# Performance work log

Hardware: AMD Instinct MI355X
Metric: run time of the kernel (lower is better)

Reference implementation:

```python
import jax, jax.numpy as jnp
import numpy as np

EPS = 1e-4

def safe_clamp(x, max_val):
    # nan -> 0, +inf -> max_val, -inf -> -max_val, then clamp to [-max_val, max_val]
    x = jnp.where(jnp.isnan(x), 0.0, x)
    x = jnp.where(jnp.isinf(x) & (x > 0), max_val, x)
    x = jnp.where(jnp.isinf(x) & (x < 0), -max_val, x)
    return jnp.clip(x, -max_val, max_val)

def setup_inputs() -> dict:
    key = jax.random.key(0)
    k1, k2 = jax.random.split(key)
    hidden_states = jax.random.normal(k1, (4, 4096, 2048), dtype=jnp.float32)
    ln_weight = jnp.ones((2048,), dtype=jnp.float32)
    ln_bias = jnp.zeros((2048,), dtype=jnp.float32)
    gate_weight = jax.random.normal(k2, (64, 2048), dtype=jnp.float32) * 0.01
    return {"hidden_states": hidden_states, "ln_weight": ln_weight,
            "ln_bias": ln_bias, "gate_weight": gate_weight}

def reference(hidden_states, ln_weight, ln_bias, gate_weight):
    B, S, H = hidden_states.shape
    top_k = 2
    x = hidden_states.reshape(-1, H)  # (N, H)
    # LayerNorm(eps=1e-5)
    mu = jnp.mean(x, axis=-1, keepdims=True)
    var = jnp.mean((x - mu) ** 2, axis=-1, keepdims=True)
    x = (x - mu) * jax.lax.rsqrt(var + 1e-5) * ln_weight + ln_bias
    x = safe_clamp(x, 50.0)
    # gate: (N, H) @ (H, E)
    router_logits = jnp.clip(x @ gate_weight.T, -10.0, 10.0)
    # eval mode: no noise
    router_probs = jnp.clip(jax.nn.softmax(router_logits, axis=-1), EPS, 1.0)
    top_k_probs, top_k_indices = jax.lax.top_k(router_probs, top_k)
    prob_sum = jnp.maximum(jnp.sum(top_k_probs, axis=-1, keepdims=True), EPS)
    top_k_probs = top_k_probs / prob_sum
    return top_k_probs, top_k_indices, router_logits
```

## Files before the change

### kernel.cpp

```cpp
#include <hip/hip_runtime.h>
#include <math.h>

#define H 2048
#define E 64
#define MR 16
#define NCH 16
#define LR 136

typedef _Float16 half8  __attribute__((ext_vector_type(8)));
typedef _Float16 half4h __attribute__((ext_vector_type(4)));
typedef float    f32x4  __attribute__((ext_vector_type(4)));

#define MFMA16(A,B,C) __builtin_amdgcn_mfma_f32_16x16x32_f16(A,B,C,0,0,0)


__global__ __launch_bounds__(256) void prep_fused(const float* __restrict__ W,
        const float* __restrict__ lnw, const float* __restrict__ lnb,
        _Float16* __restrict__ Bh, _Float16* __restrict__ Bl,
        float* __restrict__ csum, float* __restrict__ bsum) {
    {
        int idx  = blockIdx.x * 256 + threadIdx.x;
        int lane = idx & 63;
        int e  = ((idx >> 6) & 3) * 16 + (lane & 15);
        int k0 = (idx >> 8) * 32 + ((lane >> 4) << 3);
        half8 hh, ll;
        #pragma unroll
        for (int j = 0; j < 8; ++j) {
            float wf = lnw[k0 + j] * W[e * H + k0 + j];
            _Float16 h = (_Float16)wf;
            _Float16 l = (_Float16)((wf - (float)h) * 2048.0f);
            hh[j] = h; ll[j] = l;
        }
        *(half8*)&Bh[(long)idx * 8] = hh;
        *(half8*)&Bl[(long)idx * 8] = ll;
    }
    {
        __shared__ float rc[256], rb[256];
        int e = blockIdx.x, t = threadIdx.x;
        float cs = 0.f, bs = 0.f;
        #pragma unroll
        for (int j = 0; j < 8; ++j) {
            int k = t + j * 256;
            float w = W[e * H + k];
            cs += lnw[k] * w;
            bs += lnb[k] * w;
        }
        rc[t] = cs; rb[t] = bs;
        __syncthreads();
        for (int s = 128; s > 0; s >>= 1) {
            if (t < s) { rc[t] += rc[t + s]; rb[t] += rb[t + s]; }
            __syncthreads();
        }
        if (t == 0) { csum[e] = rc[0]; bsum[e] = rb[0]; }
    }
}

__global__ __launch_bounds__(256, 4) void router_kernel(
    const float* __restrict__ X, const _Float16* __restrict__ Bh,
    const _Float16* __restrict__ Bl, const float* __restrict__ csum,
    const float* __restrict__ bsum, float* __restrict__ out, int nRows)
{
    __shared__ __align__(16) _Float16 Xh[2][MR][LR];
    __shared__ __align__(16) _Float16 Xl[2][MR][LR];
    __shared__ float C2[MR][E + 4];
    __shared__ float mu_s[MR], rs_s[MR];

    const int t    = threadIdx.x;
    const int lane = t & 63;
    const int et   = t >> 6;
    const int q    = lane >> 4;
    const int ln16 = lane & 15;
    const int rowR = t >> 4;
    const int cS   = t & 15;
    const long rowBase = (long)blockIdx.x * MR;
    const long iOff = (long)nRows * 2;
    const long lOff = (long)nRows * 4;

    const float4* Xrow = (const float4*)X + (rowBase + rowR) * 512;

    float sacc = 0.f, qacc = 0.f;
    f32x4 acc0 = (f32x4)0.f;
    f32x4 acc1 = (f32x4)0.f;

    half8 WAh0, WAh1, WAh2, WAh3, WAl0, WAl1, WAl2, WAl3;
    half8 WBh0, WBh1, WBh2, WBh3, WBl0, WBl1, WBl2, WBl3;
    float4 vA0, vA1, vB0, vB1;

#define LOADW(S, c) { \
    int b0_ = ((((c) * 4 + 0) * 4 + et) * 64 + lane) * 8; \
    S##h0 = *(const half8*)&Bh[b0_];  S##l0 = *(const half8*)&Bl[b0_]; \
    int b1_ = ((((c) * 4 + 1) * 4 + et) * 64 + lane) * 8; \
    S##h1 = *(const half8*)&Bh[b1_];  S##l1 = *(const half8*)&Bl[b1_]; \
    int b2_ = ((((c) * 4 + 2) * 4 + et) * 64 + lane) * 8; \
    S##h2 = *(const half8*)&Bh[b2_];  S##l2 = *(const half8*)&Bl[b2_]; \
    int b3_ = ((((c) * 4 + 3) * 4 + et) * 64 + lane) * 8; \
    S##h3 = *(const half8*)&Bh[b3_];  S##l3 = *(const half8*)&Bl[b3_]; }

#define LOADX(S, c) { \
    S##0 = Xrow[(c) * 32 + cS]; \
    S##1 = Xrow[(c) * 32 + cS + 16]; }

#define CVT1(V, JCOL, buf) { \
    float4 v_ = (V); \
    sacc += v_.x + v_.y + v_.z + v_.w; \
    qacc += v_.x * v_.x + v_.y * v_.y + v_.z * v_.z + v_.w * v_.w; \
    _Float16 h0_ = (_Float16)v_.x, h1_ = (_Float16)v_.y, \
             h2_ = (_Float16)v_.z, h3_ = (_Float16)v_.w; \
    _Float16 l0_ = (_Float16)((v_.x - (float)h0_) * 2048.f); \
    _Float16 l1_ = (_Float16)((v_.y - (float)h1_) * 2048.f); \
    _Float16 l2_ = (_Float16)((v_.z - (float)h2_) * 2048.f); \
    _Float16 l3_ = (_Float16)((v_.w - (float)h3_) * 2048.f); \
    half4h hh_ = {h0_, h1_, h2_, h3_}; \
    half4h ll_ = {l0_, l1_, l2_, l3_}; \
    *(half4h*)&Xh[buf][rowR][(JCOL) * 4] = hh_; \
    *(half4h*)&Xl[buf][rowR][(JCOL) * 4] = ll_; }

#define CONVERT(S, buf) { CVT1(S##0, cS, buf) CVT1(S##1, cS + 16, buf) }

#define MFMAKS(Wh_, Wl_, buf, ks) { \
    half8 Ah_ = *(const half8*)&Xh[buf][ln16][(ks) * 32 + q * 8]; \
    half8 Al_ = *(const half8*)&Xl[buf][ln16][(ks) * 32 + q * 8]; \
    acc0 = MFMA16(Ah_, Wh_, acc0); \
    acc1 = MFMA16(Ah_, Wl_, acc1); \
    acc1 = MFMA16(Al_, Wh_, acc1); }

#define MFMAC(S, buf) { \
    MFMAKS(S##h0, S##l0, buf, 0) MFMAKS(S##h1, S##l1, buf, 1) \
    MFMAKS(S##h2, S##l2, buf, 2) MFMAKS(S##h3, S##l3, buf, 3) }

    {
        float4 v00 = Xrow[cS];
        float4 v01 = Xrow[cS + 16];
        LOADW(WA, 0)
        LOADX(vA, 1)
        CVT1(v00, cS, 0)
        CVT1(v01, cS + 16, 0)
    }
    __syncthreads();

    for (int c = 0; c < NCH; c += 2) {
        LOADW(WB, c + 1)
        if (c + 2 < NCH) LOADX(vB, c + 2)
        MFMAC(WA, 0)
        CONVERT(vA, 1)
        __syncthreads();

        if (c + 2 < NCH) LOADW(WA, c + 2)
        if (c + 3 < NCH) LOADX(vA, c + 3)
        MFMAC(WB, 1)
        if (c + 2 < NCH) CONVERT(vB, 0)
        __syncthreads();
    }

    {
        float s = sacc, qq = qacc;
        #pragma unroll
        for (int d = 1; d < 16; d <<= 1) {
            s  += __shfl_xor(s, d);
            qq += __shfl_xor(qq, d);
        }
        if (cS == 0) {
            float mu  = s * (1.f / H);
            float var = qq * (1.f / H) - mu * mu;
            mu_s[rowR] = mu;
            rs_s[rowR] = rsqrtf(var + 1e-5f);
        }
    }
    __syncthreads();

    {
        int n = et * 16 + ln16;
        float cs = csum[n], bs = bsum[n];
        #pragma unroll
        for (int reg = 0; reg < 4; ++reg) {
            int r = q * 4 + reg;
            float raw = acc0[reg] + acc1[reg] * (1.f / 2048.f);
            float lg = rs_s[r] * (raw - mu_s[r] * cs) + bs;
            lg = fminf(fmaxf(lg, -10.f), 10.f);
            out[lOff + (rowBase + r) * 64 + n] = lg;
            C2[r][n] = lg;
        }
    }
    __syncthreads();

    #pragma unroll
    for (int rr = 0; rr < 4; ++rr) {
        int r = et * 4 + rr;
        float l = C2[r][lane];
        float m = l;
        #pragma unroll
        for (int d = 1; d < 64; d <<= 1) m = fmaxf(m, __shfl_xor(m, d));
        float p = __expf(l - m);
        float ssum = p;
        #pragma unroll
        for (int d = 1; d < 64; d <<= 1) ssum += __shfl_xor(ssum, d);
        float prob = fminf(fmaxf(p / ssum, 1e-4f), 1.0f);

        float v1 = prob; int i1 = lane;
        #pragma unroll
        for (int d = 1; d < 64; d <<= 1) {
            float ov = __shfl_xor(v1, d);
            int   oi = __shfl_xor(i1, d);
            if (ov > v1 || (ov == v1 && oi < i1)) { v1 = ov; i1 = oi; }
        }
        float v2 = (lane == i1) ? -1.f : prob; int i2 = lane;
        #pragma unroll
        for (int d = 1; d < 64; d <<= 1) {
            float ov = __shfl_xor(v2, d);
            int   oi = __shfl_xor(i2, d);
            if (ov > v2 || (ov == v2 && oi < i2)) { v2 = ov; i2 = oi; }
        }
        if (lane == 0) {
            float ps = fmaxf(v1 + v2, 1e-4f);
            long rg_ = rowBase + r;
            out[rg_ * 2 + 0] = v1 / ps;
            out[rg_ * 2 + 1] = v2 / ps;
            out[iOff + rg_ * 2 + 0] = (float)i1;
            out[iOff + rg_ * 2 + 1] = (float)i2;
        }
    }
}

extern "C" void kernel_launch(void* const* d_in, const int* in_sizes, int n_in,
                              void* d_out, int out_size, void* d_ws, size_t ws_size,
                              hipStream_t stream) {
    const float* X   = (const float*)d_in[0];
    const float* lnw = (const float*)d_in[1];
    const float* lnb = (const float*)d_in[2];
    const float* W   = (const float*)d_in[3];
    float* outp = (float*)d_out;

    _Float16* Bh = (_Float16*)d_ws;
    _Float16* Bl = Bh + H * E;
    float* csum  = (float*)(Bl + H * E);
    float* bsum  = csum + E;

    int N = in_sizes[0] / H;

    prep_fused<<<64, 256, 0, stream>>>(W, lnw, lnb, Bh, Bl, csum, bsum);
    router_kernel<<<N / MR, 256, 0, stream>>>(X, Bh, Bl, csum, bsum, outp, N);
}
```

Before: 244.6 us.

## Load X fragments directly into registers, drop LDS staging and barriers

Each wave now reads its MFMA A-operand rows of X directly from global memory and splits them into fp16 hi/lo parts in registers, removing the LDS double buffer and per-chunk block barriers. LayerNorm statistics are reduced with cross-lane shuffles instead of shared memory. This eliminates LDS traffic and synchronization, but all four waves now redundantly load and convert the same X rows with a less coalesced row-strided pattern, and the occupancy hint is dropped.

```diff
diff --git a/kernel.cpp b/kernel.cpp
--- a/kernel.cpp
+++ b/kernel.cpp
@@ -4,11 +4,9 @@
 #define H 2048
 #define E 64
 #define MR 16
-#define NCH 16
-#define LR 136
+#define NKS 64
 
 typedef _Float16 half8  __attribute__((ext_vector_type(8)));
-typedef _Float16 half4h __attribute__((ext_vector_type(4)));
 typedef float    f32x4  __attribute__((ext_vector_type(4)));
 
 #define MFMA16(A,B,C) __builtin_amdgcn_mfma_f32_16x16x32_f16(A,B,C,0,0,0)
@@ -55,118 +53,100 @@
     }
 }
 
-__global__ __launch_bounds__(256, 4) void router_kernel(
+__global__ __launch_bounds__(256) void router_kernel(
     const float* __restrict__ X, const _Float16* __restrict__ Bh,
     const _Float16* __restrict__ Bl, const float* __restrict__ csum,
     const float* __restrict__ bsum, float* __restrict__ out, int nRows)
 {
-    __shared__ __align__(16) _Float16 Xh[2][MR][LR];
-    __shared__ __align__(16) _Float16 Xl[2][MR][LR];
     __shared__ float C2[MR][E + 4];
-    __shared__ float mu_s[MR], rs_s[MR];
 
     const int t    = threadIdx.x;
     const int lane = t & 63;
     const int et   = t >> 6;
     const int q    = lane >> 4;
     const int ln16 = lane & 15;
-    const int rowR = t >> 4;
-    const int cS   = t & 15;
     const long rowBase = (long)blockIdx.x * MR;
     const long iOff = (long)nRows * 2;
     const long lOff = (long)nRows * 4;
 
-    const float4* Xrow = (const float4*)X + (rowBase + rowR) * 512;
-
-    float sacc = 0.f, qacc = 0.f;
+    const float4* Xp = (const float4*)X + (rowBase + ln16) * 512 + q * 2;
+    const half8* BhP = (const half8*)Bh + et * 64 + lane;
+    const half8* BlP = (const half8*)Bl + et * 64 + lane;
+
     f32x4 acc0 = (f32x4)0.f;
     f32x4 acc1 = (f32x4)0.f;
-
-    half8 WAh0, WAh1, WAh2, WAh3, WAl0, WAl1, WAl2, WAl3;
-    half8 WBh0, WBh1, WBh2, WBh3, WBl0, WBl1, WBl2, WBl3;
-    float4 vA0, vA1, vB0, vB1;
-
-#define LOADW(S, c) { \
-    int b0_ = ((((c) * 4 + 0) * 4 + et) * 64 + lane) * 8; \
-    S##h0 = *(const half8*)&Bh[b0_];  S##l0 = *(const half8*)&Bl[b0_]; \
-    int b1_ = ((((c) * 4 + 1) * 4 + et) * 64 + lane) * 8; \
-    S##h1 = *(const half8*)&Bh[b1_];  S##l1 = *(const half8*)&Bl[b1_]; \
-    int b2_ = ((((c) * 4 + 2) * 4 + et) * 64 + lane) * 8; \
-    S##h2 = *(const half8*)&Bh[b2_];  S##l2 = *(const half8*)&Bl[b2_]; \
-    int b3_ = ((((c) * 4 + 3) * 4 + et) * 64 + lane) * 8; \
-    S##h3 = *(const half8*)&Bh[b3_];  S##l3 = *(const half8*)&Bl[b3_]; }
-
-#define LOADX(S, c) { \
-    S##0 = Xrow[(c) * 32 + cS]; \
-    S##1 = Xrow[(c) * 32 + cS + 16]; }
-
-#define CVT1(V, JCOL, buf) { \
-    float4 v_ = (V); \
-    sacc += v_.x + v_.y + v_.z + v_.w; \
-    qacc += v_.x * v_.x + v_.y * v_.y + v_.z * v_.z + v_.w * v_.w; \
-    _Float16 h0_ = (_Float16)v_.x, h1_ = (_Float16)v_.y, \
-             h2_ = (_Float16)v_.z, h3_ = (_Float16)v_.w; \
-    _Float16 l0_ = (_Float16)((v_.x - (float)h0_) * 2048.f); \
-    _Float16 l1_ = (_Float16)((v_.y - (float)h1_) * 2048.f); \
-    _Float16 l2_ = (_Float16)((v_.z - (float)h2_) * 2048.f); \
-    _Float16 l3_ = (_Float16)((v_.w - (float)h3_) * 2048.f); \
-    half4h hh_ = {h0_, h1_, h2_, h3_}; \
-    half4h ll_ = {l0_, l1_, l2_, l3_}; \
-    *(half4h*)&Xh[buf][rowR][(JCOL) * 4] = hh_; \
-    *(half4h*)&Xl[buf][rowR][(JCOL) * 4] = ll_; }
-
-#define CONVERT(S, buf) { CVT1(S##0, cS, buf) CVT1(S##1, cS + 16, buf) }
-
-#define MFMAKS(Wh_, Wl_, buf, ks) { \
-    half8 Ah_ = *(const half8*)&Xh[buf][ln16][(ks) * 32 + q * 8]; \
-    half8 Al_ = *(const half8*)&Xl[buf][ln16][(ks) * 32 + q * 8]; \
-    acc0 = MFMA16(Ah_, Wh_, acc0); \
-    acc1 = MFMA16(Ah_, Wl_, acc1); \
-    acc1 = MFMA16(Al_, Wh_, acc1); }
-
-#define MFMAC(S, buf) { \
-    MFMAKS(S##h0, S##l0, buf, 0) MFMAKS(S##h1, S##l1, buf, 1) \
-    MFMAKS(S##h2, S##l2, buf, 2) MFMAKS(S##h3, S##l3, buf, 3) }
-
-    {
-        float4 v00 = Xrow[cS];
-        float4 v01 = Xrow[cS + 16];
-        LOADW(WA, 0)
-        LOADX(vA, 1)
-        CVT1(v00, cS, 0)
-        CVT1(v01, cS + 16, 0)
-    }
-    __syncthreads();
-
-    for (int c = 0; c < NCH; c += 2) {
-        LOADW(WB, c + 1)
-        if (c + 2 < NCH) LOADX(vB, c + 2)
-        MFMAC(WA, 0)
-        CONVERT(vA, 1)
-        __syncthreads();
-
-        if (c + 2 < NCH) LOADW(WA, c + 2)
-        if (c + 3 < NCH) LOADX(vA, c + 3)
-        MFMAC(WB, 1)
-        if (c + 2 < NCH) CONVERT(vB, 0)
-        __syncthreads();
-    }
-
-    {
-        float s = sacc, qq = qacc;
-        #pragma unroll
-        for (int d = 1; d < 16; d <<= 1) {
-            s  += __shfl_xor(s, d);
-            qq += __shfl_xor(qq, d);
-        }
-        if (cS == 0) {
-            float mu  = s * (1.f / H);
-            float var = qq * (1.f / H) - mu * mu;
-            mu_s[rowR] = mu;
-            rs_s[rowR] = rsqrtf(var + 1e-5f);
-        }
-    }
-    __syncthreads();
+    float sacc = 0.f, qacc = 0.f;
+
+#define CVT8(V0, V1, AH, AL) { \
+    float4 v0_ = (V0), v1_ = (V1); \
+    sacc += v0_.x + v0_.y + v0_.z + v0_.w + v1_.x + v1_.y + v1_.z + v1_.w; \
+    qacc += v0_.x*v0_.x + v0_.y*v0_.y + v0_.z*v0_.z + v0_.w*v0_.w \
+          + v1_.x*v1_.x + v1_.y*v1_.y + v1_.z*v1_.z + v1_.w*v1_.w; \
+    _Float16 h0_ = (_Float16)v0_.x, h1_ = (_Float16)v0_.y, \
+             h2_ = (_Float16)v0_.z, h3_ = (_Float16)v0_.w, \
+             h4_ = (_Float16)v1_.x, h5_ = (_Float16)v1_.y, \
+             h6_ = (_Float16)v1_.z, h7_ = (_Float16)v1_.w; \
+    AH[0] = h0_; AH[1] = h1_; AH[2] = h2_; AH[3] = h3_; \
+    AH[4] = h4_; AH[5] = h5_; AH[6] = h6_; AH[7] = h7_; \
+    AL[0] = (_Float16)((v0_.x - (float)h0_) * 2048.f); \
+    AL[1] = (_Float16)((v0_.y - (float)h1_) * 2048.f); \
+    AL[2] = (_Float16)((v0_.z - (float)h2_) * 2048.f); \
+    AL[3] = (_Float16)((v0_.w - (float)h3_) * 2048.f); \
+    AL[4] = (_Float16)((v1_.x - (float)h4_) * 2048.f); \
+    AL[5] = (_Float16)((v1_.y - (float)h5_) * 2048.f); \
+    AL[6] = (_Float16)((v1_.z - (float)h6_) * 2048.f); \
+    AL[7] = (_Float16)((v1_.w - (float)h7_) * 2048.f); }
+
+    float4 xA0 = Xp[0], xA1 = Xp[1];
+    float4 xB0 = Xp[8], xB1 = Xp[9];
+    half8 wAh = BhP[0], wAl = BlP[0];
+    half8 wBh, wBl;
+
+    for (int ks = 0; ks < NKS; ks += 2) {
+        {
+            wBh = BhP[(ks + 1) * 256];
+            wBl = BlP[(ks + 1) * 256];
+            half8 Ah, Al;
+            CVT8(xA0, xA1, Ah, Al)
+            if (ks + 2 < NKS) {
+                xA0 = Xp[(ks + 2) * 8];
+                xA1 = Xp[(ks + 2) * 8 + 1];
+            }
+            acc0 = MFMA16(Ah, wAh, acc0);
+            acc1 = MFMA16(Ah, wAl, acc1);
+            acc1 = MFMA16(Al, wAh, acc1);
+        }
+        {
+            if (ks + 2 < NKS) {
+                wAh = BhP[(ks + 2) * 256];
+                wAl = BlP[(ks + 2) * 256];
+            }
+            half8 Ah, Al;
+            CVT8(xB0, xB1, Ah, Al)
+            if (ks + 3 < NKS) {
+                xB0 = Xp[(ks + 3) * 8];
+                xB1 = Xp[(ks + 3) * 8 + 1];
+            }
+            acc0 = MFMA16(Ah, wBh, acc0);
+            acc1 = MFMA16(Ah, wBl, acc1);
+            acc1 = MFMA16(Al, wBh, acc1);
+        }
+    }
+
+    sacc += __shfl_xor(sacc, 16);
+    sacc += __shfl_xor(sacc, 32);
+    qacc += __shfl_xor(qacc, 16);
+    qacc += __shfl_xor(qacc, 32);
+    float mu4[4], rs4[4];
+    #pragma unroll
+    for (int reg = 0; reg < 4; ++reg) {
+        int r = q * 4 + reg;
+        float s  = __shfl(sacc, r);
+        float qq = __shfl(qacc, r);
+        float mu = s * (1.f / H);
+        mu4[reg] = mu;
+        rs4[reg] = rsqrtf(qq * (1.f / H) - mu * mu + 1e-5f);
+    }
 
     {
         int n = et * 16 + ln16;
@@ -175,7 +155,7 @@
         for (int reg = 0; reg < 4; ++reg) {
             int r = q * 4 + reg;
             float raw = acc0[reg] + acc1[reg] * (1.f / 2048.f);
-            float lg = rs_s[r] * (raw - mu_s[r] * cs) + bs;
+            float lg = rs4[reg] * (raw - mu4[reg] * cs) + bs;
             lg = fminf(fmaxf(lg, -10.f), 10.f);
             out[lOff + (rowBase + r) * 64 + n] = lg;
             C2[r][n] = lg;
```

Result: faster. 236.3 us (-3.4%).
